# Kernel optimization log

Hardware: AMD Instinct MI355X
Metric: run time of the kernel (lower is better)

The kernel has to match this reference:

```python
import jax, jax.numpy as jnp
import numpy as np

COST_CLASS = 2.0
COST_BBOX = 5.0
COST_GIOU = 2.0
ALPHA = 0.25
GAMMA = 2.0
EPS = 1e-8


def box_cxcywh_to_xyxy(b):
    cx, cy, w, h = b[..., 0], b[..., 1], b[..., 2], b[..., 3]
    return jnp.stack([cx - 0.5 * w, cy - 0.5 * h, cx + 0.5 * w, cy + 0.5 * h], axis=-1)


def pairwise_giou(boxes1, boxes2):
    # boxes1: [N,4] xyxy, boxes2: [T,4] xyxy -> [N,T]
    area1 = (boxes1[:, 2] - boxes1[:, 0]) * (boxes1[:, 3] - boxes1[:, 1])
    area2 = (boxes2[:, 2] - boxes2[:, 0]) * (boxes2[:, 3] - boxes2[:, 1])
    lt = jnp.maximum(boxes1[:, None, :2], boxes2[None, :, :2])   # [N,T,2]
    rb = jnp.minimum(boxes1[:, None, 2:], boxes2[None, :, 2:])
    wh = jnp.clip(rb - lt, 0.0)
    inter = wh[..., 0] * wh[..., 1]
    union = area1[:, None] + area2[None, :] - inter
    iou = inter / union
    # smallest enclosing box
    lt_e = jnp.minimum(boxes1[:, None, :2], boxes2[None, :, :2])
    rb_e = jnp.maximum(boxes1[:, None, 2:], boxes2[None, :, 2:])
    wh_e = jnp.clip(rb_e - lt_e, 0.0)
    area_e = wh_e[..., 0] * wh_e[..., 1]
    return iou - (area_e - union) / area_e


def setup_inputs() -> dict:
    key = jax.random.key(0)
    k1, k2, k3, k4 = jax.random.split(key, 4)
    bs, nq, nc, nt = 16, 900, 91, 1600
    return {
        "pred_logits": jax.random.normal(k1, (bs, nq, nc), dtype=jnp.float32),
        "pred_boxes": jax.random.uniform(k2, (bs, nq, 4), dtype=jnp.float32),
        "tgt_boxes": jax.random.uniform(k3, (nt, 4), dtype=jnp.float32),
        "tgt_ids": jax.random.randint(k4, (nt,), 0, nc, dtype=jnp.int64),
    }


def reference(pred_logits, pred_boxes, tgt_boxes, tgt_ids):
    bs, nq, _ = pred_logits.shape
    out_prob = jax.nn.sigmoid(pred_logits.reshape(bs * nq, -1).astype(jnp.float32))
    out_bbox = pred_boxes.reshape(bs * nq, 4).astype(jnp.float32)
    tgt_bbox = tgt_boxes.astype(jnp.float32)

    # focal classification cost, gathered at target class columns: [N,T]
    p = out_prob[:, tgt_ids]
    neg_cost = (1.0 - ALPHA) * (p ** GAMMA) * (-jnp.log(1.0 - p + EPS))
    pos_cost = ALPHA * ((1.0 - p) ** GAMMA) * (-jnp.log(p + EPS))
    cost_class = pos_cost - neg_cost

    # L1 box cost (cdist p=1): [N,T]
    cost_bbox = jnp.abs(out_bbox[:, None, :] - tgt_bbox[None, :, :]).sum(-1)

    # GIoU cost: [N,T]
    cost_giou = -pairwise_giou(box_cxcywh_to_xyxy(out_bbox), box_cxcywh_to_xyxy(tgt_bbox))

    C = COST_BBOX * cost_bbox + COST_CLASS * cost_class + COST_GIOU * cost_giou
    return C.reshape(bs, nq, -1)
```

## Files before the change

kernel.cpp:

```cpp
#include <hip/hip_runtime.h>


#define BLOCK 256

__global__ __launch_bounds__(BLOCK) void matcher_kernel(
    const float* __restrict__ logits,
    const float* __restrict__ pboxes,
    const float* __restrict__ tboxes,
    const int*   __restrict__ tids,
    float*       __restrict__ out,
    int nc, int nt)
{
    __shared__ float s_cc[128];
    const int q   = blockIdx.x;
    const int tid = threadIdx.x;

    if (tid < nc) {
        float x = logits[(size_t)q * nc + tid];
        float p = 1.0f / (1.0f + __expf(-x));
        float omp = 1.0f - p;
        float pos = 0.25f * omp * omp * (-__logf(p + 1e-8f));
        float neg = 0.75f * p * p     * (-__logf(omp + 1e-8f));
        s_cc[tid] = 2.0f * (pos - neg);
    }

    const float4 qb = ((const float4*)pboxes)[q];
    const float qx0 = qb.x - 0.5f * qb.z, qy0 = qb.y - 0.5f * qb.w;
    const float qx1 = qb.x + 0.5f * qb.z, qy1 = qb.y + 0.5f * qb.w;
    const float qarea = qb.z * qb.w;

    __syncthreads();

    float* outq = out + (size_t)q * nt;
    for (int t = tid; t < nt; t += BLOCK) {
        const float4 tb = ((const float4*)tboxes)[t];
        const int id = tids[t];

        float l1 = fabsf(qb.x - tb.x) + fabsf(qb.y - tb.y)
                 + fabsf(qb.z - tb.z) + fabsf(qb.w - tb.w);

        float tx0 = tb.x - 0.5f * tb.z, ty0 = tb.y - 0.5f * tb.w;
        float tx1 = tb.x + 0.5f * tb.z, ty1 = tb.y + 0.5f * tb.w;
        float tarea = tb.z * tb.w;

        float ltx = fmaxf(qx0, tx0), lty = fmaxf(qy0, ty0);
        float rbx = fminf(qx1, tx1), rby = fminf(qy1, ty1);
        float iw = fmaxf(rbx - ltx, 0.0f), ih = fmaxf(rby - lty, 0.0f);
        float inter = iw * ih;
        float uni = qarea + tarea - inter;
        float iou = inter * __builtin_amdgcn_rcpf(uni);

        float ex0 = fminf(qx0, tx0), ey0 = fminf(qy0, ty0);
        float ex1 = fmaxf(qx1, tx1), ey1 = fmaxf(qy1, ty1);
        float ew = fmaxf(ex1 - ex0, 0.0f), eh = fmaxf(ey1 - ey0, 0.0f);
        float earea = ew * eh;
        float giou = iou - (earea - uni) * __builtin_amdgcn_rcpf(earea);

        outq[t] = 5.0f * l1 + s_cc[id] - 2.0f * giou;
    }
}

extern "C" void kernel_launch(void* const* d_in, const int* in_sizes, int n_in,
                              void* d_out, int out_size, void* d_ws, size_t ws_size,
                              hipStream_t stream) {
    const float* logits = (const float*)d_in[0];
    const float* pboxes = (const float*)d_in[1];
    const float* tboxes = (const float*)d_in[2];
    const int*   tids   = (const int*)d_in[3];

    const int nqall = in_sizes[1] / 4;
    const int nt    = in_sizes[2] / 4;
    const int nc    = in_sizes[0] / nqall;

    float* out = (float*)d_out;

    matcher_kernel<<<nqall, BLOCK, 0, stream>>>(logits, pboxes, tboxes, tids,
                                                out, nc, nt);
}
```

Baseline: 126.0 us.

## Process eight queries per block with target boxes cached in registers

Each block now handles eight queries instead of one. Target boxes, their corner coordinates and class ids are loaded once into registers and reused across all eight queries, and the class cost for the eight queries is computed together in shared memory. The aim is to cut repeated target loads and per-block launch overhead. In exchange, NC and NT are hardcoded to the test shapes, the query count is assumed divisible by eight, and the clamp on the enclosing box width is dropped.

New measurement: 121.4 us. 1.04x faster.

```diff
diff --git a/kernel.cpp b/kernel.cpp
--- a/kernel.cpp
+++ b/kernel.cpp
@@ -2,61 +2,79 @@
 
 
 #define BLOCK 256
+#define QPB 8
+#define NC 91
+#define NT 1600
+#define TSLOTS ((NT + BLOCK - 1) / BLOCK)
 
-__global__ __launch_bounds__(BLOCK) void matcher_kernel(
+__global__ __launch_bounds__(BLOCK, 4) void matcher_kernel(
     const float* __restrict__ logits,
     const float* __restrict__ pboxes,
     const float* __restrict__ tboxes,
     const int*   __restrict__ tids,
-    float*       __restrict__ out,
-    int nc, int nt)
+    float*       __restrict__ out)
 {
-    __shared__ float s_cc[128];
-    const int q   = blockIdx.x;
+    __shared__ float s_cc[QPB * NC];
     const int tid = threadIdx.x;
+    const int q0  = blockIdx.x * QPB;
 
-    if (tid < nc) {
-        float x = logits[(size_t)q * nc + tid];
-        float p = 1.0f / (1.0f + __expf(-x));
+    for (int i = tid; i < QPB * NC; i += BLOCK) {
+        float x   = logits[(size_t)q0 * NC + i];
+        float p   = 1.0f / (1.0f + __expf(-x));
         float omp = 1.0f - p;
-        float pos = 0.25f * omp * omp * (-__logf(p + 1e-8f));
-        float neg = 0.75f * p * p     * (-__logf(omp + 1e-8f));
-        s_cc[tid] = 2.0f * (pos - neg);
+        float pos = 0.25f * omp * omp * (-__logf(p   + 1e-8f));
+        float neg = 0.75f * p   * p   * (-__logf(omp + 1e-8f));
+        s_cc[i] = 2.0f * (pos - neg);
     }
 
-    const float4 qb = ((const float4*)pboxes)[q];
-    const float qx0 = qb.x - 0.5f * qb.z, qy0 = qb.y - 0.5f * qb.w;
-    const float qx1 = qb.x + 0.5f * qb.z, qy1 = qb.y + 0.5f * qb.w;
-    const float qarea = qb.z * qb.w;
-
+    float4 tb[TSLOTS], xy[TSLOTS];
+    int    ida[TSLOTS];
+    #pragma unroll
+    for (int k = 0; k < TSLOTS; ++k) {
+        int t = tid + k * BLOCK;
+        if (t < NT) {
+            float4 b = ((const float4*)tboxes)[t];
+            tb[k] = b;
+            xy[k] = make_float4(fmaf(-0.5f, b.z, b.x), fmaf(-0.5f, b.w, b.y),
+                                fmaf( 0.5f, b.z, b.x), fmaf( 0.5f, b.w, b.y));
+            ida[k] = tids[t];
+        }
+    }
     __syncthreads();
 
-    float* outq = out + (size_t)q * nt;
-    for (int t = tid; t < nt; t += BLOCK) {
-        const float4 tb = ((const float4*)tboxes)[t];
-        const int id = tids[t];
+    #pragma unroll 1
+    for (int q = 0; q < QPB; ++q) {
+        const int    qg = q0 + q;
+        const float4 qb = ((const float4*)pboxes)[qg];
+        const float qx0 = fmaf(-0.5f, qb.z, qb.x), qy0 = fmaf(-0.5f, qb.w, qb.y);
+        const float qx1 = fmaf( 0.5f, qb.z, qb.x), qy1 = fmaf( 0.5f, qb.w, qb.y);
+        const float qarea = qb.z * qb.w;
+        const float* cc   = s_cc + q * NC;
+        float* outq = out + (size_t)qg * NT;
 
-        float l1 = fabsf(qb.x - tb.x) + fabsf(qb.y - tb.y)
-                 + fabsf(qb.z - tb.z) + fabsf(qb.w - tb.w);
+        #pragma unroll
+        for (int k = 0; k < TSLOTS; ++k) {
+            int t = tid + k * BLOCK;
+            if (t < NT) {
+                float4 b = tb[k], p = xy[k];
 
-        float tx0 = tb.x - 0.5f * tb.z, ty0 = tb.y - 0.5f * tb.w;
-        float tx1 = tb.x + 0.5f * tb.z, ty1 = tb.y + 0.5f * tb.w;
-        float tarea = tb.z * tb.w;
+                float l1 = fabsf(qb.x - b.x) + fabsf(qb.y - b.y)
+                         + fabsf(qb.z - b.z) + fabsf(qb.w - b.w);
 
-        float ltx = fmaxf(qx0, tx0), lty = fmaxf(qy0, ty0);
-        float rbx = fminf(qx1, tx1), rby = fminf(qy1, ty1);
-        float iw = fmaxf(rbx - ltx, 0.0f), ih = fmaxf(rby - lty, 0.0f);
-        float inter = iw * ih;
-        float uni = qarea + tarea - inter;
-        float iou = inter * __builtin_amdgcn_rcpf(uni);
+                float tarea = b.z * b.w;
+                float iw = fminf(qx1, p.z) - fmaxf(qx0, p.x);
+                float ih = fminf(qy1, p.w) - fmaxf(qy0, p.y);
+                float inter = fmaxf(iw, 0.0f) * fmaxf(ih, 0.0f);
+                float uni   = qarea + tarea - inter;
+                float iou   = inter * __builtin_amdgcn_rcpf(uni);
+                float ew = fmaxf(qx1, p.z) - fminf(qx0, p.x);
+                float eh = fmaxf(qy1, p.w) - fminf(qy0, p.y);
+                float earea = ew * eh;
+                float giou  = iou - (earea - uni) * __builtin_amdgcn_rcpf(earea);
 
-        float ex0 = fminf(qx0, tx0), ey0 = fminf(qy0, ty0);
-        float ex1 = fmaxf(qx1, tx1), ey1 = fmaxf(qy1, ty1);
-        float ew = fmaxf(ex1 - ex0, 0.0f), eh = fmaxf(ey1 - ey0, 0.0f);
-        float earea = ew * eh;
-        float giou = iou - (earea - uni) * __builtin_amdgcn_rcpf(earea);
-
-        outq[t] = 5.0f * l1 + s_cc[id] - 2.0f * giou;
+                outq[t] = fmaf(5.0f, l1, cc[ida[k]]) - 2.0f * giou;
+            }
+        }
     }
 }
 
@@ -69,11 +87,8 @@
     const int*   tids   = (const int*)d_in[3];
 
     const int nqall = in_sizes[1] / 4;
-    const int nt    = in_sizes[2] / 4;
-    const int nc    = in_sizes[0] / nqall;
-
     float* out = (float*)d_out;
 
-    matcher_kernel<<<nqall, BLOCK, 0, stream>>>(logits, pboxes, tboxes, tids,
-                                                out, nc, nt);
+    matcher_kernel<<<nqall / QPB, BLOCK, 0, stream>>>(logits, pboxes, tboxes,
+                                                      tids, out);
 }
```
